# Kernel tuning notes

Hardware: AMD Instinct MI355X
Metric: run time of the kernel (lower is better)

Reference implementation:

```python
import jax, jax.numpy as jnp
import numpy as np

E = 1024
H = 16
HD = E // H  # head_dim = 64
N, T, S = 2, 2048, 2048
NEG = -1e9


def setup_inputs() -> dict:
    key = jax.random.key(0)
    ks = jax.random.split(key, 12)
    s = 0.02
    inp = {
        "query": jax.random.normal(ks[0], (N, T, E), jnp.float32),
        "key": jax.random.normal(ks[1], (N, S, E), jnp.float32),
        "value": jax.random.normal(ks[2], (N, S, E), jnp.float32),
        # causal mask: mask[i, j] == 0 means target i cannot attend to source j
        "attn_mask": jnp.tril(jnp.ones((T, S), jnp.float32)),
        "pad_mask": jnp.zeros((N, S), bool),
        "Wq": jax.random.normal(ks[3], (E, E), jnp.float32) * s,
        "bq": jnp.zeros((E,), jnp.float32),
        "Wk": jax.random.normal(ks[4], (E, E), jnp.float32) * s,
        "bk": jnp.zeros((E,), jnp.float32),
        "Wv": jax.random.normal(ks[5], (E, E), jnp.float32) * s,
        "bv": jnp.zeros((E,), jnp.float32),
        "Wp": jax.random.normal(ks[6], (E, E), jnp.float32) * s,
        "bp": jnp.zeros((E,), jnp.float32),
    }
    return inp


def reference(query, key, value, attn_mask, pad_mask, Wq, bq, Wk, bk, Wv, bv, Wp, bp):
    n, t, _ = query.shape
    _, srcl, _ = key.shape
    # Linear projections (torch Linear: x @ W.T + b), split into heads
    Q = (query @ Wq.T + bq).reshape(n, t, H, HD).transpose(0, 2, 1, 3)      # (N,H,T,HD)
    K = (key @ Wk.T + bk).reshape(n, srcl, H, HD).transpose(0, 2, 1, 3)     # (N,H,S,HD)
    V = (value @ Wv.T + bv).reshape(n, srcl, H, HD).transpose(0, 2, 1, 3)   # (N,H,S,HD)
    scores = jnp.einsum("nhtd,nhsd->nhts", Q, K) / jnp.sqrt(jnp.float32(HD))
    scores = jnp.where(pad_mask[:, None, None, :], NEG, scores)
    scores = jnp.where(attn_mask[None, None, :, :] == 0, NEG, scores)
    att = jax.nn.softmax(scores, axis=-1)  # dropout=0 (eval)
    Y = jnp.einsum("nhts,nhsd->nhtd", att, V)
    Y = Y.transpose(0, 2, 1, 3).reshape(n, t, E)
    return Y @ Wp.T + bp
```

## Files before the change

kernel.cpp:

```cpp
#include <hip/hip_runtime.h>
#include <hip/hip_bf16.h>

#define E_  1024
#define H_  16
#define HD_ 64
#define NB  2
#define T_  2048
#define S_  2048
#define KD  1024

#define QSCALE 0.18033688011112042f

typedef __attribute__((ext_vector_type(8))) short short8;
typedef __attribute__((ext_vector_type(4))) short short4v;
typedef __attribute__((ext_vector_type(4))) float floatx4;

static __device__ __forceinline__ unsigned short f2bf(float f) {
    unsigned int u = __float_as_uint(f);
    unsigned int r = (u + 0x7FFFu + ((u >> 16) & 1u)) >> 16;
    return (unsigned short)r;
}

static __device__ __forceinline__ unsigned short f2bf_fast(float f) {
    return (unsigned short)((__float_as_uint(f) + 0x8000u) >> 16);
}

static __device__ __forceinline__ floatx4 mfma16(short8 a, short8 b, floatx4 c) {
    return __builtin_amdgcn_mfma_f32_16x16x32_bf16(a, b, c, 0, 0, 0);
}

static __device__ __forceinline__ void gload_lds16(const void* g, void* l) {
    __builtin_amdgcn_global_load_lds(
        (const __attribute__((address_space(1))) unsigned int*)g,
        (__attribute__((address_space(3))) unsigned int*)l, 16, 0, 0);
}

#define VMCNT0_BARRIER() do {                                   \
    __builtin_amdgcn_sched_barrier(0);                          \
    asm volatile("s_waitcnt vmcnt(0)" ::: "memory");            \
    __builtin_amdgcn_s_barrier();                               \
    __builtin_amdgcn_sched_barrier(0);                          \
} while (0)

#define VMCNT4_BARRIER() do {                                   \
    __builtin_amdgcn_sched_barrier(0);                          \
    asm volatile("s_waitcnt vmcnt(4)" ::: "memory");            \
    __builtin_amdgcn_s_barrier();                               \
    __builtin_amdgcn_sched_barrier(0);                          \
} while (0)

__global__ __launch_bounds__(256) void conv_all_kernel(
    const float* __restrict__ wq, const float* __restrict__ wk,
    const float* __restrict__ wv, const float* __restrict__ wp,
    const float* __restrict__ qi, const float* __restrict__ ki,
    const float* __restrict__ vi,
    unsigned short* __restrict__ Wb, unsigned short* __restrict__ Xb)
{
    const int NW4 = 1 << 18;
    const int NX4 = 1 << 20;
    const int TOT = 4 * NW4 + 3 * NX4;
    int idx = blockIdx.x * 256 + threadIdx.x;
    for (int i4 = idx; i4 < TOT; i4 += 262144) {
        const float* s; unsigned short* d; int off4;
        float sc = 1.0f;
        if (i4 < 4 * NW4) {
            int seg = i4 >> 18; off4 = i4 & (NW4 - 1);
            s = (seg == 0) ? wq : (seg == 1) ? wk : (seg == 2) ? wv : wp;
            d = Wb + ((size_t)seg << 20);
            if (seg == 0) sc = QSCALE;
        } else {
            int j = i4 - 4 * NW4; int seg = j >> 20; off4 = j & (NX4 - 1);
            s = (seg == 0) ? qi : (seg == 1) ? ki : vi;
            d = Xb + ((size_t)seg << 22);
        }
        float4 v = *(const float4*)&s[(size_t)off4 * 4];
        short4v b;
        b[0] = (short)f2bf(v.x * sc); b[1] = (short)f2bf(v.y * sc);
        b[2] = (short)f2bf(v.z * sc); b[3] = (short)f2bf(v.w * sc);
        *(short4v*)&d[(size_t)off4 * 4] = b;
    }
}

__global__ __launch_bounds__(256) void proj_qkv_kernel(
    const unsigned short* __restrict__ Xb, const unsigned short* __restrict__ Wb,
    const float* __restrict__ bq, const float* __restrict__ bk, const float* __restrict__ bv,
    unsigned short* __restrict__ Qh, unsigned short* __restrict__ K2, unsigned short* __restrict__ V2)
{
    const int z = blockIdx.z;
    const unsigned short* X = Xb + ((size_t)z << 22);
    const unsigned short* W = Wb + ((size_t)z << 20);
    const float* bias = (z == 0) ? bq : (z == 1) ? bk : bv;
    unsigned short* dst = (z == 0) ? Qh : (z == 1) ? K2 : V2;

    __shared__ unsigned short Sm[32768];

    const int tid  = threadIdx.x;
    const int lane = tid & 63;
    const int w    = tid >> 6;
    const int wm   = w >> 1, wn = w & 1;
    const int m0   = blockIdx.x * 128;
    const int e0   = blockIdx.y * 128;
    const int l15  = lane & 15, lg = lane >> 4;

    floatx4 acc[4][4];
#pragma unroll
    for (int mi = 0; mi < 4; ++mi)
#pragma unroll
        for (int ni = 0; ni < 4; ++ni)
            acc[mi][ni] = (floatx4){0.f, 0.f, 0.f, 0.f};

    const int rc = lane >> 3;
    const int sl = (lane & 7) ^ rc;

#pragma unroll
    for (int jj = 0; jj < 4; ++jj) {
        int c = w * 4 + jj;
        int row = c * 8 + rc;
        gload_lds16(&X[(size_t)(m0 + row) * KD + sl * 8], &Sm[c * 512]);
        gload_lds16(&W[(size_t)(e0 + row) * KD + sl * 8], &Sm[16384 + c * 512]);
    }
    VMCNT0_BARRIER();

    for (int kt = 0; kt < 16; ++kt) {
        const int cur = (kt & 1) * 8192;
        const int nxt = ((kt + 1) & 1) * 8192;
        const unsigned short* Ac = Sm + cur;
        const unsigned short* Bc = Sm + 16384 + cur;
        unsigned short* An = Sm + nxt;
        unsigned short* Bn = Sm + 16384 + nxt;
        const int k0n = (kt + 1) * 64;

        if (kt < 15) {
#pragma unroll
            for (int jj = 0; jj < 4; ++jj) {
                int c = w * 4 + jj;
                int row = c * 8 + rc;
                gload_lds16(&X[(size_t)(m0 + row) * KD + k0n + sl * 8], &An[c * 512]);
            }
        }
        {
            short8 af[4], bf[4];
#pragma unroll
            for (int mi = 0; mi < 4; ++mi) {
                int r_ = wm * 64 + mi * 16 + l15;
                af[mi] = *(const short8*)&Ac[r_ * 64 + ((lg ^ (r_ & 7)) << 3)];
            }
#pragma unroll
            for (int ni = 0; ni < 4; ++ni) {
                int r_ = wn * 64 + ni * 16 + l15;
                bf[ni] = *(const short8*)&Bc[r_ * 64 + ((lg ^ (r_ & 7)) << 3)];
            }
#pragma unroll
            for (int mi = 0; mi < 4; ++mi)
#pragma unroll
                for (int ni = 0; ni < 4; ++ni)
                    acc[mi][ni] = mfma16(af[mi], bf[ni], acc[mi][ni]);
        }
        if (kt < 15) {
#pragma unroll
            for (int jj = 0; jj < 4; ++jj) {
                int c = w * 4 + jj;
                int row = c * 8 + rc;
                gload_lds16(&W[(size_t)(e0 + row) * KD + k0n + sl * 8], &Bn[c * 512]);
            }
        }
        {
            short8 af[4], bf[4];
#pragma unroll
            for (int mi = 0; mi < 4; ++mi) {
                int r_ = wm * 64 + mi * 16 + l15;
                af[mi] = *(const short8*)&Ac[r_ * 64 + (((4 + lg) ^ (r_ & 7)) << 3)];
            }
#pragma unroll
            for (int ni = 0; ni < 4; ++ni) {
                int r_ = wn * 64 + ni * 16 + l15;
                bf[ni] = *(const short8*)&Bc[r_ * 64 + (((4 + lg) ^ (r_ & 7)) << 3)];
            }
#pragma unroll
            for (int mi = 0; mi < 4; ++mi)
#pragma unroll
                for (int ni = 0; ni < 4; ++ni)
                    acc[mi][ni] = mfma16(af[mi], bf[ni], acc[mi][ni]);
        }
        VMCNT0_BARRIER();
    }

    if (z != 2) {
#pragma unroll
        for (int mi = 0; mi < 4; ++mi)
#pragma unroll
            for (int ni = 0; ni < 4; ++ni) {
                int col = wn * 64 + ni * 16 + l15;
                float bb = bias[e0 + col];
                if (z == 0) bb *= QSCALE;
#pragma unroll
                for (int r = 0; r < 4; ++r) {
                    int row = wm * 64 + mi * 16 + (lg << 2) + r;
                    Sm[row * 128 + (col ^ ((row & 7) << 3))] =
                        f2bf(acc[mi][ni][r] + bb);
                }
            }
    } else {
#pragma unroll
        for (int mi = 0; mi < 4; ++mi)
#pragma unroll
            for (int ni = 0; ni < 4; ++ni) {
                int col = wn * 64 + ni * 16 + l15;
                float bb = bias[e0 + col];
                int rb = wm * 64 + mi * 16 + (lg << 2);
                short4v sv;
#pragma unroll
                for (int r = 0; r < 4; ++r) sv[r] = (short)f2bf(acc[mi][ni][r] + bb);
                *(short4v*)&Sm[col * 128 + (rb ^ ((col & 7) << 3))] = sv;
            }
    }
    __syncthreads();

    {
        const int r0 = tid >> 1;
        const int cb2 = (tid & 1) * 64;
#pragma unroll
        for (int j = 0; j < 8; ++j) {
            int c = cb2 + j * 8;
            short8 v = *(const short8*)&Sm[r0 * 128 + (c ^ ((r0 & 7) << 3))];
            if (z == 0) {
                int m = m0 + r0, nn = m >> 11, t = m & (T_ - 1);
                int e = e0 + c, hh = e >> 6, d = e & 63;
                size_t hb = (size_t)(nn * H_ + hh) * (T_ * HD_);
                *(short8*)&dst[hb + (size_t)t * HD_ + d] = v;
            } else if (z == 1) {
                int m = m0 + r0, nn = m >> 11, t = m & (T_ - 1);
                int e = e0 + c, hh = e >> 6, d = e & 63;
                size_t hb = (size_t)(nn * H_ + hh) * (T_ * HD_);
                *(short8*)&dst[hb + (t >> 6) * 4096 + (t & 63) * 64 +
                               (((d >> 3) ^ (t & 7)) << 3)] = v;
            } else {
                int e = e0 + r0, hh = e >> 6, d = e & 63;
                int m = m0 + c, nn = m >> 11, t = m & (T_ - 1);
                size_t hb = (size_t)(nn * H_ + hh) * (T_ * HD_);
                *(short8*)&dst[hb + (t >> 6) * 4096 + d * 64 +
                               ((((t >> 3) & 7) ^ (d & 7)) << 3)] = v;
            }
        }
    }
}

__global__ __launch_bounds__(256) void flash_attn_kernel(
    const unsigned short* __restrict__ Qh, const unsigned short* __restrict__ K2,
    const unsigned short* __restrict__ V2, unsigned short* __restrict__ Y)
{
    const int linear = blockIdx.x;
    const int xcd = linear & 7;
    const int idx = linear >> 3;
    const int nh  = xcd * 4 + (idx & 3);
    const int n   = nh >> 4, h = nh & 15;
    const int qt  = 31 - (idx >> 2);
    const int q0  = qt * 64;
    const int nkv = (qt + 2) >> 1;

    const int tid = threadIdx.x, lane = tid & 63, w = tid >> 6;
    const int l15 = lane & 15, lg = lane >> 4;

    const unsigned short* Qp = Qh + (size_t)(n * H_ + h) * (T_ * HD_);
    const unsigned short* Kt = K2 + (size_t)(n * H_ + h) * (T_ * HD_);
    const unsigned short* Vt = V2 + (size_t)(n * H_ + h) * (T_ * HD_);

    __shared__ unsigned short Ks_l[8192];
    __shared__ unsigned short VT_l[8192];
    __shared__ unsigned short Ps[64][136];

    const int prow = w * 16 + lg * 4;
    const int arow = w * 16 + l15;
    const int sw7  = l15 & 7;

    short8 qf[2];
#pragma unroll
    for (int ks = 0; ks < 2; ++ks)
        qf[ks] = *(const short8*)&Qp[(size_t)(q0 + arow) * HD_ + ks * 32 + lg * 8];

    floatx4 o[4];
    float lacc[4];
#pragma unroll
    for (int hi = 0; hi < 4; ++hi) o[hi] = (floatx4){0.f, 0.f, 0.f, 0.f};
#pragma unroll
    for (int r = 0; r < 4; ++r) lacc[r] = 0.f;

#pragma unroll
    for (int j = 0; j < 4; ++j) {
        int c = w * 4 + j;
        gload_lds16(&Kt[c * 512 + lane * 8], &Ks_l[c * 512]);
    }
#pragma unroll
    for (int j = 0; j < 4; ++j) {
        int c = w * 4 + j;
        gload_lds16(&Vt[c * 512 + lane * 8], &VT_l[c * 512]);
    }
    VMCNT4_BARRIER();

    for (int kb2 = 0; kb2 < nkv; ++kb2) {
        floatx4 sa[8];
#pragma unroll
        for (int ni = 0; ni < 8; ++ni) sa[ni] = (floatx4){0.f, 0.f, 0.f, 0.f};
        __builtin_amdgcn_s_setprio(1);
#pragma unroll
        for (int ks = 0; ks < 2; ++ks) {
            short8 kf[8];
#pragma unroll
            for (int ni = 0; ni < 8; ++ni)
                kf[ni] = *(const short8*)
                    &Ks_l[(ni * 16 + l15) * 64 + (((ks * 4 + lg) ^ sw7) << 3)];
#pragma unroll
            for (int ni = 0; ni < 8; ++ni)
                sa[ni] = mfma16(qf[ks], kf[ni], sa[ni]);
        }
        __builtin_amdgcn_s_setprio(0);

        const bool diag = (kb2 == nkv - 1);
        const int sbase = kb2 * 128;
        float pv[8][4];
#pragma unroll
        for (int ni = 0; ni < 8; ++ni)
#pragma unroll
            for (int r = 0; r < 4; ++r) {
                float e = __builtin_amdgcn_exp2f(sa[ni][r]);
                if (diag && (sbase + ni * 16 + l15 > q0 + prow + r)) e = 0.f;
                pv[ni][r] = e;
            }
#pragma unroll
        for (int r = 0; r < 4; ++r)
            lacc[r] += ((pv[0][r] + pv[1][r]) + (pv[2][r] + pv[3][r]))
                     + ((pv[4][r] + pv[5][r]) + (pv[6][r] + pv[7][r]));

#pragma unroll
        for (int ni = 0; ni < 8; ++ni)
#pragma unroll
            for (int r = 0; r < 4; ++r)
                Ps[prow + r][(ni * 16 + l15) ^ (lg << 3)] = f2bf_fast(pv[ni][r]);

        VMCNT0_BARRIER();
        if (kb2 + 1 < nkv) {
            const unsigned short* Ksrc = Kt + (kb2 + 1) * 8192;
#pragma unroll
            for (int j = 0; j < 4; ++j) {
                int c = w * 4 + j;
                gload_lds16(&Ksrc[c * 512 + lane * 8], &Ks_l[c * 512]);
            }
        }

        __builtin_amdgcn_s_setprio(1);
#pragma unroll
        for (int ksp = 0; ksp < 4; ++ksp) {
            short8 pa = *(const short8*)
                &Ps[arow][(ksp * 32 + lg * 8) ^ ((l15 >> 2) << 3)];
            short8 vt[4];
#pragma unroll
            for (int hi = 0; hi < 4; ++hi)
                vt[hi] = *(const short8*)
                    &VT_l[(ksp >> 1) * 4096 + (hi * 16 + l15) * 64 +
                          ((((ksp & 1) * 4 + lg) ^ sw7) << 3)];
#pragma unroll
            for (int hi = 0; hi < 4; ++hi)
                o[hi] = mfma16(pa, vt[hi], o[hi]);
        }
        __builtin_amdgcn_s_setprio(0);

        __builtin_amdgcn_s_barrier();
        if (kb2 + 1 < nkv) {
            const unsigned short* Vsrc = Vt + (kb2 + 1) * 8192;
#pragma unroll
            for (int j = 0; j < 4; ++j) {
                int c = w * 4 + j;
                gload_lds16(&Vsrc[c * 512 + lane * 8], &VT_l[c * 512]);
            }
        }
        VMCNT4_BARRIER();
    }

    float linv[4];
#pragma unroll
    for (int r = 0; r < 4; ++r) {
        float l = lacc[r];
#pragma unroll
        for (int off = 1; off < 16; off <<= 1)
            l += __shfl_xor(l, off);
        linv[r] = 1.0f / l;
    }

#pragma unroll
    for (int hi = 0; hi < 4; ++hi) {
        int col = hi * 16 + l15;
#pragma unroll
        for (int r = 0; r < 4; ++r) {
            int t = q0 + prow + r;
            Y[((size_t)n * T_ + t) * E_ + h * HD_ + col] =
                f2bf(o[hi][r] * linv[r]);
        }
    }
}

__global__ __launch_bounds__(256) void proj_out_kernel(
    const unsigned short* __restrict__ Yb, const unsigned short* __restrict__ Wpb,
    const float* __restrict__ bp, float* __restrict__ out)
{
    __shared__ unsigned short Sm[32768];

    const int tid  = threadIdx.x;
    const int lane = tid & 63;
    const int w    = tid >> 6;
    const int wm   = w >> 1, wn = w & 1;
    const int m0   = blockIdx.x * 128;
    const int e0   = blockIdx.y * 128;
    const int l15  = lane & 15, lg = lane >> 4;

    floatx4 acc[4][4];
#pragma unroll
    for (int mi = 0; mi < 4; ++mi)
#pragma unroll
        for (int ni = 0; ni < 4; ++ni)
            acc[mi][ni] = (floatx4){0.f, 0.f, 0.f, 0.f};

    const int rc = lane >> 3;
    const int sl = (lane & 7) ^ rc;

#pragma unroll
    for (int jj = 0; jj < 4; ++jj) {
        int c = w * 4 + jj;
        int row = c * 8 + rc;
        gload_lds16(&Yb[(size_t)(m0 + row) * E_ + sl * 8], &Sm[c * 512]);
        gload_lds16(&Wpb[(size_t)(e0 + row) * E_ + sl * 8], &Sm[16384 + c * 512]);
    }
    VMCNT0_BARRIER();

    for (int kt = 0; kt < 16; ++kt) {
        const int cur = (kt & 1) * 8192;
        const int nxt = ((kt + 1) & 1) * 8192;
        const unsigned short* Ac = Sm + cur;
        const unsigned short* Bc = Sm + 16384 + cur;
        unsigned short* An = Sm + nxt;
        unsigned short* Bn = Sm + 16384 + nxt;
        const int k0n = (kt + 1) * 64;

        if (kt < 15) {
#pragma unroll
            for (int jj = 0; jj < 4; ++jj) {
                int c = w * 4 + jj;
                int row = c * 8 + rc;
                gload_lds16(&Yb[(size_t)(m0 + row) * E_ + k0n + sl * 8], &An[c * 512]);
            }
        }
        {
            short8 af[4], bf[4];
#pragma unroll
            for (int mi = 0; mi < 4; ++mi) {
                int r_ = wm * 64 + mi * 16 + l15;
                af[mi] = *(const short8*)&Ac[r_ * 64 + ((lg ^ (r_ & 7)) << 3)];
            }
#pragma unroll
            for (int ni = 0; ni < 4; ++ni) {
                int r_ = wn * 64 + ni * 16 + l15;
                bf[ni] = *(const short8*)&Bc[r_ * 64 + ((lg ^ (r_ & 7)) << 3)];
            }
#pragma unroll
            for (int mi = 0; mi < 4; ++mi)
#pragma unroll
                for (int ni = 0; ni < 4; ++ni)
                    acc[mi][ni] = mfma16(af[mi], bf[ni], acc[mi][ni]);
        }
        if (kt < 15) {
#pragma unroll
            for (int jj = 0; jj < 4; ++jj) {
                int c = w * 4 + jj;
                int row = c * 8 + rc;
                gload_lds16(&Wpb[(size_t)(e0 + row) * E_ + k0n + sl * 8], &Bn[c * 512]);
            }
        }
        {
            short8 af[4], bf[4];
#pragma unroll
            for (int mi = 0; mi < 4; ++mi) {
                int r_ = wm * 64 + mi * 16 + l15;
                af[mi] = *(const short8*)&Ac[r_ * 64 + (((4 + lg) ^ (r_ & 7)) << 3)];
            }
#pragma unroll
            for (int ni = 0; ni < 4; ++ni) {
                int r_ = wn * 64 + ni * 16 + l15;
                bf[ni] = *(const short8*)&Bc[r_ * 64 + (((4 + lg) ^ (r_ & 7)) << 3)];
            }
#pragma unroll
            for (int mi = 0; mi < 4; ++mi)
#pragma unroll
                for (int ni = 0; ni < 4; ++ni)
                    acc[mi][ni] = mfma16(af[mi], bf[ni], acc[mi][ni]);
        }
        VMCNT0_BARRIER();
    }

#pragma unroll
    for (int mi = 0; mi < 4; ++mi) {
#pragma unroll
        for (int ni = 0; ni < 4; ++ni) {
            int e = e0 + wn * 64 + ni * 16 + l15;
            float bb = bp[e];
#pragma unroll
            for (int r = 0; r < 4; ++r) {
                int m = m0 + wm * 64 + mi * 16 + (lg << 2) + r;
                out[(size_t)m * E_ + e] = acc[mi][ni][r] + bb;
            }
        }
    }
}

extern "C" void kernel_launch(void* const* d_in, const int* in_sizes, int n_in,
                              void* d_out, int out_size, void* d_ws, size_t ws_size,
                              hipStream_t stream) {
    const float* query = (const float*)d_in[0];
    const float* key_  = (const float*)d_in[1];
    const float* value = (const float*)d_in[2];
    const float* Wq = (const float*)d_in[5];
    const float* bq = (const float*)d_in[6];
    const float* Wk = (const float*)d_in[7];
    const float* bk = (const float*)d_in[8];
    const float* Wv = (const float*)d_in[9];
    const float* bv = (const float*)d_in[10];
    const float* Wp = (const float*)d_in[11];
    const float* bp = (const float*)d_in[12];
    float* out = (float*)d_out;

    const size_t P = (size_t)NB * H_ * T_ * HD_;
    unsigned short* Qh  = (unsigned short*)d_ws;
    unsigned short* K2  = Qh + P;
    unsigned short* V2  = K2 + P;
    unsigned short* Wb  = V2 + P;
    unsigned short* Xb  = Wb + (4u << 20);
    unsigned short* Yb  = Xb;
    unsigned short* Wpb = Wb + (3u << 20);

    conv_all_kernel<<<dim3(1024), 256, 0, stream>>>(
        Wq, Wk, Wv, Wp, query, key_, value, Wb, Xb);
    proj_qkv_kernel<<<dim3(32, 8, 3), 256, 0, stream>>>(
        Xb, Wb, bq, bk, bv, Qh, K2, V2);
    flash_attn_kernel<<<dim3(1024), 256, 0, stream>>>(Qh, K2, V2, Yb);
    proj_out_kernel<<<dim3(32, 8), 256, 0, stream>>>(Yb, Wpb, bp, out);
}
```

Measured before the change: 108.9 us.

## Use 128-row query tiles with 8 warps and pair causal tiles per block

The flash attention kernel now runs 512-thread blocks covering 128 query rows. Each block processes two query tiles, one short and one long (pb and 15-pb), so every block does the same amount of causal work. The grid drops from 1024 to 256 blocks, and each K/V tile loaded into LDS is shared by twice as many query rows. In exchange, there are fewer blocks to fill the CUs, the two tiles in a block run one after the other, and diagonal tiles do more masked work since the block size is now 128.

```diff
diff --git a/kernel.cpp b/kernel.cpp
--- a/kernel.cpp
+++ b/kernel.cpp
@@ -42,9 +42,9 @@
     __builtin_amdgcn_sched_barrier(0);                          \
 } while (0)
 
-#define VMCNT4_BARRIER() do {                                   \
+#define VMCNT2_BARRIER() do {                                   \
     __builtin_amdgcn_sched_barrier(0);                          \
-    asm volatile("s_waitcnt vmcnt(4)" ::: "memory");            \
+    asm volatile("s_waitcnt vmcnt(2)" ::: "memory");            \
     __builtin_amdgcn_s_barrier();                               \
     __builtin_amdgcn_sched_barrier(0);                          \
 } while (0)
@@ -245,18 +245,15 @@
     }
 }
 
-__global__ __launch_bounds__(256) void flash_attn_kernel(
+__global__ __launch_bounds__(512) void flash_attn_kernel(
     const unsigned short* __restrict__ Qh, const unsigned short* __restrict__ K2,
     const unsigned short* __restrict__ V2, unsigned short* __restrict__ Y)
 {
-    const int linear = blockIdx.x;
-    const int xcd = linear & 7;
-    const int idx = linear >> 3;
+    const int xcd = blockIdx.x & 7;
+    const int idx = blockIdx.x >> 3;
     const int nh  = xcd * 4 + (idx & 3);
     const int n   = nh >> 4, h = nh & 15;
-    const int qt  = 31 - (idx >> 2);
-    const int q0  = qt * 64;
-    const int nkv = (qt + 2) >> 1;
+    const int pb  = idx >> 2;
 
     const int tid = threadIdx.x, lane = tid & 63, w = tid >> 6;
     const int l15 = lane & 15, lg = lane >> 4;
@@ -267,133 +264,129 @@
 
     __shared__ unsigned short Ks_l[8192];
     __shared__ unsigned short VT_l[8192];
-    __shared__ unsigned short Ps[64][136];
+    __shared__ unsigned short Ps[128][136];
 
     const int prow = w * 16 + lg * 4;
     const int arow = w * 16 + l15;
     const int sw7  = l15 & 7;
-
-    short8 qf[2];
-#pragma unroll
-    for (int ks = 0; ks < 2; ++ks)
-        qf[ks] = *(const short8*)&Qp[(size_t)(q0 + arow) * HD_ + ks * 32 + lg * 8];
-
-    floatx4 o[4];
-    float lacc[4];
-#pragma unroll
-    for (int hi = 0; hi < 4; ++hi) o[hi] = (floatx4){0.f, 0.f, 0.f, 0.f};
-#pragma unroll
-    for (int r = 0; r < 4; ++r) lacc[r] = 0.f;
-
-#pragma unroll
-    for (int j = 0; j < 4; ++j) {
-        int c = w * 4 + j;
-        gload_lds16(&Kt[c * 512 + lane * 8], &Ks_l[c * 512]);
-    }
-#pragma unroll
-    for (int j = 0; j < 4; ++j) {
-        int c = w * 4 + j;
-        gload_lds16(&Vt[c * 512 + lane * 8], &VT_l[c * 512]);
-    }
-    VMCNT4_BARRIER();
-
-    for (int kb2 = 0; kb2 < nkv; ++kb2) {
-        floatx4 sa[8];
-#pragma unroll
-        for (int ni = 0; ni < 8; ++ni) sa[ni] = (floatx4){0.f, 0.f, 0.f, 0.f};
-        __builtin_amdgcn_s_setprio(1);
-#pragma unroll
-        for (int ks = 0; ks < 2; ++ks) {
-            short8 kf[8];
+    const int c0   = w * 2, c1 = w * 2 + 1;
+
+#pragma unroll
+    for (int side = 0; side < 2; ++side) {
+        const int qt  = side ? (15 - pb) : pb;
+        const int q0  = qt * 128;
+        const int nkv = qt + 1;
+
+        short8 qf[2];
+#pragma unroll
+        for (int ks = 0; ks < 2; ++ks)
+            qf[ks] = *(const short8*)&Qp[(size_t)(q0 + arow) * HD_ + ks * 32 + lg * 8];
+
+        floatx4 o[4];
+        float lacc[4];
+#pragma unroll
+        for (int hi = 0; hi < 4; ++hi) o[hi] = (floatx4){0.f, 0.f, 0.f, 0.f};
+#pragma unroll
+        for (int r = 0; r < 4; ++r) lacc[r] = 0.f;
+
+        gload_lds16(&Kt[c0 * 512 + lane * 8], &Ks_l[c0 * 512]);
+        gload_lds16(&Kt[c1 * 512 + lane * 8], &Ks_l[c1 * 512]);
+        gload_lds16(&Vt[c0 * 512 + lane * 8], &VT_l[c0 * 512]);
+        gload_lds16(&Vt[c1 * 512 + lane * 8], &VT_l[c1 * 512]);
+        VMCNT2_BARRIER();
+
+        for (int kb2 = 0; kb2 < nkv; ++kb2) {
+            floatx4 sa[8];
+#pragma unroll
+            for (int ni = 0; ni < 8; ++ni) sa[ni] = (floatx4){0.f, 0.f, 0.f, 0.f};
+            __builtin_amdgcn_s_setprio(1);
+#pragma unroll
+            for (int ks = 0; ks < 2; ++ks) {
+                short8 kf[8];
+#pragma unroll
+                for (int ni = 0; ni < 8; ++ni)
+                    kf[ni] = *(const short8*)
+                        &Ks_l[(ni * 16 + l15) * 64 + (((ks * 4 + lg) ^ sw7) << 3)];
+#pragma unroll
+                for (int ni = 0; ni < 8; ++ni)
+                    sa[ni] = mfma16(qf[ks], kf[ni], sa[ni]);
+            }
+            __builtin_amdgcn_s_setprio(0);
+
+            const bool diag = (kb2 == nkv - 1);
+            const int sbase = kb2 * 128;
+            float pv[8][4];
 #pragma unroll
             for (int ni = 0; ni < 8; ++ni)
-                kf[ni] = *(const short8*)
-                    &Ks_l[(ni * 16 + l15) * 64 + (((ks * 4 + lg) ^ sw7) << 3)];
+#pragma unroll
+                for (int r = 0; r < 4; ++r) {
+                    float e = __builtin_amdgcn_exp2f(sa[ni][r]);
+                    if (diag && (sbase + ni * 16 + l15 > q0 + prow + r)) e = 0.f;
+                    pv[ni][r] = e;
+                }
+#pragma unroll
+            for (int r = 0; r < 4; ++r)
+                lacc[r] += ((pv[0][r] + pv[1][r]) + (pv[2][r] + pv[3][r]))
+                         + ((pv[4][r] + pv[5][r]) + (pv[6][r] + pv[7][r]));
+
 #pragma unroll
             for (int ni = 0; ni < 8; ++ni)
-                sa[ni] = mfma16(qf[ks], kf[ni], sa[ni]);
-        }
-        __builtin_amdgcn_s_setprio(0);
-
-        const bool diag = (kb2 == nkv - 1);
-        const int sbase = kb2 * 128;
-        float pv[8][4];
-#pragma unroll
-        for (int ni = 0; ni < 8; ++ni)
+#pragma unroll
+                for (int r = 0; r < 4; ++r)
+                    Ps[prow + r][(ni * 16 + l15) ^ (lg << 3)] = f2bf_fast(pv[ni][r]);
+
+            VMCNT0_BARRIER();
+            if (kb2 + 1 < nkv) {
+                const unsigned short* Ksrc = Kt + (kb2 + 1) * 8192;
+                gload_lds16(&Ksrc[c0 * 512 + lane * 8], &Ks_l[c0 * 512]);
+                gload_lds16(&Ksrc[c1 * 512 + lane * 8], &Ks_l[c1 * 512]);
+            }
+
+            __builtin_amdgcn_s_setprio(1);
+#pragma unroll
+            for (int ksp = 0; ksp < 4; ++ksp) {
+                short8 pa = *(const short8*)
+                    &Ps[arow][(ksp * 32 + lg * 8) ^ ((l15 >> 2) << 3)];
+                short8 vt[4];
+#pragma unroll
+                for (int hi = 0; hi < 4; ++hi)
+                    vt[hi] = *(const short8*)
+                        &VT_l[(ksp >> 1) * 4096 + (hi * 16 + l15) * 64 +
+                              ((((ksp & 1) * 4 + lg) ^ sw7) << 3)];
+#pragma unroll
+                for (int hi = 0; hi < 4; ++hi)
+                    o[hi] = mfma16(pa, vt[hi], o[hi]);
+            }
+            __builtin_amdgcn_s_setprio(0);
+
+            __builtin_amdgcn_s_barrier();
+            if (kb2 + 1 < nkv) {
+                const unsigned short* Vsrc = Vt + (kb2 + 1) * 8192;
+                gload_lds16(&Vsrc[c0 * 512 + lane * 8], &VT_l[c0 * 512]);
+                gload_lds16(&Vsrc[c1 * 512 + lane * 8], &VT_l[c1 * 512]);
+            }
+            VMCNT2_BARRIER();
+        }
+
+        float linv[4];
+#pragma unroll
+        for (int r = 0; r < 4; ++r) {
+            float l = lacc[r];
+#pragma unroll
+            for (int off = 1; off < 16; off <<= 1)
+                l += __shfl_xor(l, off);
+            linv[r] = 1.0f / l;
+        }
+
+#pragma unroll
+        for (int hi = 0; hi < 4; ++hi) {
+            int col = hi * 16 + l15;
 #pragma unroll
             for (int r = 0; r < 4; ++r) {
-                float e = __builtin_amdgcn_exp2f(sa[ni][r]);
-                if (diag && (sbase + ni * 16 + l15 > q0 + prow + r)) e = 0.f;
-                pv[ni][r] = e;
-            }
-#pragma unroll
-        for (int r = 0; r < 4; ++r)
-            lacc[r] += ((pv[0][r] + pv[1][r]) + (pv[2][r] + pv[3][r]))
-                     + ((pv[4][r] + pv[5][r]) + (pv[6][r] + pv[7][r]));
-
-#pragma unroll
-        for (int ni = 0; ni < 8; ++ni)
-#pragma unroll
-            for (int r = 0; r < 4; ++r)
-                Ps[prow + r][(ni * 16 + l15) ^ (lg << 3)] = f2bf_fast(pv[ni][r]);
-
-        VMCNT0_BARRIER();
-        if (kb2 + 1 < nkv) {
-            const unsigned short* Ksrc = Kt + (kb2 + 1) * 8192;
-#pragma unroll
-            for (int j = 0; j < 4; ++j) {
-                int c = w * 4 + j;
-                gload_lds16(&Ksrc[c * 512 + lane * 8], &Ks_l[c * 512]);
-            }
-        }
-
-        __builtin_amdgcn_s_setprio(1);
-#pragma unroll
-        for (int ksp = 0; ksp < 4; ++ksp) {
-            short8 pa = *(const short8*)
-                &Ps[arow][(ksp * 32 + lg * 8) ^ ((l15 >> 2) << 3)];
-            short8 vt[4];
-#pragma unroll
-            for (int hi = 0; hi < 4; ++hi)
-                vt[hi] = *(const short8*)
-                    &VT_l[(ksp >> 1) * 4096 + (hi * 16 + l15) * 64 +
-                          ((((ksp & 1) * 4 + lg) ^ sw7) << 3)];
-#pragma unroll
-            for (int hi = 0; hi < 4; ++hi)
-                o[hi] = mfma16(pa, vt[hi], o[hi]);
-        }
-        __builtin_amdgcn_s_setprio(0);
-
-        __builtin_amdgcn_s_barrier();
-        if (kb2 + 1 < nkv) {
-            const unsigned short* Vsrc = Vt + (kb2 + 1) * 8192;
-#pragma unroll
-            for (int j = 0; j < 4; ++j) {
-                int c = w * 4 + j;
-                gload_lds16(&Vsrc[c * 512 + lane * 8], &VT_l[c * 512]);
-            }
-        }
-        VMCNT4_BARRIER();
-    }
-
-    float linv[4];
-#pragma unroll
-    for (int r = 0; r < 4; ++r) {
-        float l = lacc[r];
-#pragma unroll
-        for (int off = 1; off < 16; off <<= 1)
-            l += __shfl_xor(l, off);
-        linv[r] = 1.0f / l;
-    }
-
-#pragma unroll
-    for (int hi = 0; hi < 4; ++hi) {
-        int col = hi * 16 + l15;
-#pragma unroll
-        for (int r = 0; r < 4; ++r) {
-            int t = q0 + prow + r;
-            Y[((size_t)n * T_ + t) * E_ + h * HD_ + col] =
-                f2bf(o[hi][r] * linv[r]);
+                int t = q0 + prow + r;
+                Y[((size_t)n * T_ + t) * E_ + h * HD_ + col] =
+                    f2bf(o[hi][r] * linv[r]);
+            }
         }
     }
 }
@@ -539,6 +532,6 @@
         Wq, Wk, Wv, Wp, query, key_, value, Wb, Xb);
     proj_qkv_kernel<<<dim3(32, 8, 3), 256, 0, stream>>>(
         Xb, Wb, bq, bk, bv, Qh, K2, V2);
-    flash_attn_kernel<<<dim3(1024), 256, 0, stream>>>(Qh, K2, V2, Yb);
+    flash_attn_kernel<<<dim3(256), 512, 0, stream>>>(Qh, K2, V2, Yb);
     proj_out_kernel<<<dim3(32, 8), 256, 0, stream>>>(Yb, Wpb, bp, out);
 }
```

After: 109.0 us. No clear change (+0.0%).
